# Performance work log

Hardware: AMD Instinct MI355X
Metric: run time of the kernel (lower is better)

## Reference

```python
import jax, jax.numpy as jnp
import numpy as np

S = 7          # number of slots
B = 8192       # batch
D = 1024       # input_dim
E = 256        # slot_embedding_dim
H = 512        # rnn_hidden_dim
SH = 256       # slot_hidden_dim
V = 100        # labels per slot (uniform)


def _lstm_cell(x, h, c, W_ih, W_hh, b_ih, b_hh):
    # PyTorch LSTMCell: gates ordered i, f, g, o
    gates = x @ W_ih.T + b_ih + h @ W_hh.T + b_hh
    i, f, g, o = jnp.split(gates, 4, axis=-1)
    i = jax.nn.sigmoid(i); f = jax.nn.sigmoid(f)
    g = jnp.tanh(g); o = jax.nn.sigmoid(o)
    c_new = f * c + i * g
    h_new = o * jnp.tanh(c_new)
    return h_new, c_new


def setup_inputs() -> dict:
    key = jax.random.key(0)
    ks = jax.random.split(key, 24)
    sc = 0.05
    D0 = D + E  # layer-0 input size
    inp = {
        'inputs': jax.random.normal(ks[0], (B, D), jnp.float32),
        'labels': jax.random.randint(ks[1], (S - 1, B), 0, V),
        'start': jax.random.normal(ks[2], (E,), jnp.float32),
        'emb': jax.random.normal(ks[3], (S - 1, V, E), jnp.float32) * sc,
        # layer 0 (input size D0)
        'W_ih0': jax.random.normal(ks[4], (S, 4 * H, D0), jnp.float32) * sc,
        'W_hh0': jax.random.normal(ks[5], (S, 4 * H, H), jnp.float32) * sc,
        'b_ih0': jax.random.normal(ks[6], (S, 4 * H), jnp.float32) * sc,
        'b_hh0': jax.random.normal(ks[7], (S, 4 * H), jnp.float32) * sc,
        'hwN_W0': jax.random.normal(ks[8], (S, H, D0 + H), jnp.float32) * sc,
        'hwN_b0': jax.random.normal(ks[9], (S, H), jnp.float32) * sc,
        'hwL_W0': jax.random.normal(ks[10], (S, H, D0), jnp.float32) * sc,
        # layer 1 (input size H)
        'W_ih1': jax.random.normal(ks[11], (S, 4 * H, H), jnp.float32) * sc,
        'W_hh1': jax.random.normal(ks[12], (S, 4 * H, H), jnp.float32) * sc,
        'b_ih1': jax.random.normal(ks[13], (S, 4 * H), jnp.float32) * sc,
        'b_hh1': jax.random.normal(ks[14], (S, 4 * H), jnp.float32) * sc,
        'hwN_W1': jax.random.normal(ks[15], (S, H, H + H), jnp.float32) * sc,
        'hwN_b1': jax.random.normal(ks[16], (S, H), jnp.float32) * sc,
        'hwL_W1': jax.random.normal(ks[17], (S, H, H), jnp.float32) * sc,
        # slot hidden + classifier
        'sh_W': jax.random.normal(ks[18], (S, SH, H), jnp.float32) * sc,
        'sh_b': jax.random.normal(ks[19], (S, SH), jnp.float32) * sc,
        'pred_W': jax.random.normal(ks[20], (S, V, SH), jnp.float32) * sc,
        'pred_b': jax.random.normal(ks[21], (S, V), jnp.float32) * sc,
    }
    return inp


def reference(inputs, labels, start, emb,
              W_ih0, W_hh0, b_ih0, b_hh0, hwN_W0, hwN_b0, hwL_W0,
              W_ih1, W_hh1, b_ih1, b_hh1, hwN_W1, hwN_b1, hwL_W1,
              sh_W, sh_b, pred_W, pred_b):
    bsz = inputs.shape[0]
    cur_emb = jnp.broadcast_to(start[None, :], (bsz, E))
    h0 = jnp.zeros((bsz, H), inputs.dtype); c0 = jnp.zeros((bsz, H), inputs.dtype)
    h1 = jnp.zeros((bsz, H), inputs.dtype); c1 = jnp.zeros((bsz, H), inputs.dtype)
    logits_all = []
    for i in range(S):  # slots are a short, structurally distinct recurrence
        x = jnp.concatenate([inputs, cur_emb], axis=-1)  # [B, D+E]
        # layer 0
        h0, c0 = _lstm_cell(x, h0, c0, W_ih0[i], W_hh0[i], b_ih0[i], b_hh0[i])
        gate = jax.nn.sigmoid(jnp.concatenate([x, h0], -1) @ hwN_W0[i].T + hwN_b0[i])
        cur = gate * h0 + (1.0 - gate) * (x @ hwL_W0[i].T)
        # layer 1
        h1, c1 = _lstm_cell(cur, h1, c1, W_ih1[i], W_hh1[i], b_ih1[i], b_hh1[i])
        gate1 = jax.nn.sigmoid(jnp.concatenate([cur, h1], -1) @ hwN_W1[i].T + hwN_b1[i])
        # (highway output of last layer feeds nothing further for this slot)
        _ = gate1 * h1 + (1.0 - gate1) * (cur @ hwL_W1[i].T)
        hidden = jax.nn.relu(h1 @ sh_W[i].T + sh_b[i])     # [B, SH]
        logits_all.append(hidden @ pred_W[i].T + pred_b[i])  # [B, V]
        if i < S - 1:
            cur_emb = emb[i][labels[i]]  # teacher-forced embedding lookup
    return jnp.stack(logits_all, axis=0)  # [S, B, V]
```

## Files before the change

kernel.cpp:

```cpp
#include <hip/hip_runtime.h>

#define SLOTS 7
#define BATCH 8192

typedef __attribute__((ext_vector_type(8))) __bf16 bf16x8;
typedef __attribute__((ext_vector_type(4))) float f32x4;

__device__ __forceinline__ void gl_lds16(const __bf16* g, __bf16* l) {
  __builtin_amdgcn_global_load_lds(
      (const __attribute__((address_space(1))) void*)g,
      (__attribute__((address_space(3))) void*)l, 16, 0, 0);
}

__device__ __forceinline__ float sigmoidf_(float x) {
  return 1.f / (1.f + __expf(-x));
}
__device__ __forceinline__ float tanhf_(float x) {
  float xc = fminf(fmaxf(x, -15.f), 15.f);
  float e = __expf(2.f * xc);
  return (e - 1.f) / (e + 1.f);
}

#define VMW(n) asm volatile("s_waitcnt vmcnt(" #n ")" ::: "memory")
#define BARF()                       \
  __builtin_amdgcn_s_barrier();      \
  asm volatile("" ::: "memory")

__global__ void __launch_bounds__(512, 2)
gemm8p(const __bf16* __restrict__ A, int lda,
       const __bf16* __restrict__ Bw, int ldb,
       const float* __restrict__ b_ih, const float* __restrict__ b_hh,
       float* __restrict__ cst, __bf16* __restrict__ hout, int hld, int hoff,
       float* __restrict__ auxw,
       int N, int NT, int NTaux, int Nreal) {
  extern __shared__ __bf16 lds[];
#define LDSH(b, s) (lds + (((b) << 2) + (s)) * 8192)
  const int tid = threadIdx.x;
  const int w = tid >> 6, lane = tid & 63;
  const int wr = w >> 2, wc = w & 3;
  const int ln = lane & 15, lh = lane >> 4;
  const int nbx = N >> 8;
  const int NB = gridDim.x;
  const int bid = blockIdx.x;
  const int wg = (bid & 7) * (NB >> 3) + (bid >> 3);
  const int bx = wg % nbx, by = wg / nbx;
  const int blockM = by << 8, blockN = bx << 8;
  const int nt = (blockN < Nreal) ? NT : NTaux;

  f32x4 acc[8][4];
#pragma unroll
  for (int i = 0; i < 8; ++i)
#pragma unroll
    for (int j = 0; j < 4; ++j) acc[i][j] = (f32x4){0.f, 0.f, 0.f, 0.f};

  auto stage = [&](int nb, int s, int kt) {
    const __bf16* base = (s & 1) ? Bw : A;
    const int ld = (s & 1) ? ldb : lda;
    const int rb = (s & 1) ? blockN : blockM;
    const int kh = s >> 1;
#pragma unroll
    for (int j = 0; j < 2; ++j) {
      const int c = j * 512 + w * 64 + lane;
      const int row = c >> 2;
      const int blklog = (c & 3) ^ ((c >> 3) & 3);
      const __bf16* src =
          base + (size_t)(rb + row) * ld + kt * 64 + kh * 32 + blklog * 8;
      gl_lds16(src, LDSH(nb, s) + j * 4096 + w * 512);
    }
  };

  bf16x8 a[8], bb[2];
  const int swz = ((lh ^ ((ln >> 1) & 3)) << 3);

#define RDA(slot)                                                            \
  {                                                                          \
    const __bf16* ap = LDSH(buf, slot);                                      \
    _Pragma("unroll") for (int mi = 0; mi < 8; ++mi) a[mi] =                 \
        *(const bf16x8*)&ap[(wr * 128 + mi * 16 + ln) * 32 + swz];           \
  }
#define RDB(slot, nh)                                                        \
  {                                                                          \
    const __bf16* bp = LDSH(buf, slot);                                      \
    _Pragma("unroll") for (int ni = 0; ni < 2; ++ni) bb[ni] =                \
        *(const bf16x8*)&bp[(wc * 64 + (nh)*32 + ni * 16 + ln) * 32 + swz];  \
  }
#define MFMA16(nh)                                                           \
  __builtin_amdgcn_s_setprio(1);                                             \
  _Pragma("unroll") for (int mi = 0; mi < 8; ++mi)                           \
      _Pragma("unroll") for (int ni = 0; ni < 2; ++ni)                       \
          acc[mi][(nh)*2 + ni] = __builtin_amdgcn_mfma_f32_16x16x32_bf16(    \
              a[mi], bb[ni], acc[mi][(nh)*2 + ni], 0, 0, 0);                 \
  __builtin_amdgcn_s_setprio(0);

#pragma unroll
  for (int s4 = 0; s4 < 4; ++s4) stage(0, s4, 0);
  VMW(4);
  BARF();

  int buf = 0;
  for (int t = 0; t < nt; ++t) {
    const int nb = buf ^ 1;
    const bool hn = (t + 1 < nt);
    RDA(0); RDB(1, 0);
    if (hn) stage(nb, 0, t + 1);
    MFMA16(0);
    RDB(1, 1);
    if (hn) stage(nb, 1, t + 1);
    MFMA16(1);
    if (hn) { VMW(4); } else { VMW(0); }
    BARF();
    RDA(2); RDB(3, 0);
    if (hn) stage(nb, 2, t + 1);
    MFMA16(0);
    RDB(3, 1);
    if (hn) stage(nb, 3, t + 1);
    MFMA16(1);
    if (hn) { VMW(4); }
    BARF();
    buf = nb;
  }
#undef RDA
#undef RDB
#undef MFMA16
#undef LDSH

  const int row0 = blockM + wr * 128 + (lh << 2);
  if (blockN < Nreal) {
    const int h = (((blockN >> 6) + wc) << 4) + ln;
    const float bs0 = b_ih[h] + b_hh[h];
    const float bs1 = b_ih[512 + h] + b_hh[512 + h];
    const float bs2 = b_ih[1024 + h] + b_hh[1024 + h];
    const float bs3 = b_ih[1536 + h] + b_hh[1536 + h];
#pragma unroll
    for (int mi = 0; mi < 8; ++mi)
#pragma unroll
      for (int r = 0; r < 4; ++r) {
        const int row = row0 + mi * 16 + r;
        float gi = sigmoidf_(acc[mi][0][r] + bs0);
        float gf = sigmoidf_(acc[mi][1][r] + bs1);
        float gg = tanhf_(acc[mi][2][r] + bs2);
        float go = sigmoidf_(acc[mi][3][r] + bs3);
        const size_t ci = (size_t)row * 512 + h;
        float cn = gf * cst[ci] + gi * gg;
        cst[ci] = cn;
        hout[(size_t)row * hld + hoff + h] = (__bf16)(go * tanhf_(cn));
      }
  } else {
#pragma unroll
    for (int mi = 0; mi < 8; ++mi)
#pragma unroll
      for (int n = 0; n < 4; ++n) {
        const int col = blockN - Nreal + wc * 64 + n * 16 + ln;
#pragma unroll
        for (int r = 0; r < 4; ++r)
          auxw[(size_t)(row0 + mi * 16 + r) * 1024 + col] = acc[mi][n][r];
      }
  }
}

template <int MODE>
__global__ void __launch_bounds__(256)
gemm_bt(const __bf16* __restrict__ A, int lda,
        const __bf16* __restrict__ Bw, int ldb,
        void* __restrict__ Cout, int ldc,
        const float* __restrict__ bias,
        const float* __restrict__ auxr,
        __bf16* __restrict__ hout, int hld, int hoff,
        const __bf16* __restrict__ hsrc,
        int M, int N, int K, int Nreal) {
  __shared__ __align__(16) __bf16 As[2][128 * 32];
  __shared__ __align__(16) __bf16 Bs[2][128 * 32];
  const int w = threadIdx.x >> 6;
  const int lane = threadIdx.x & 63;
  const int wr = w >> 1, wc = w & 1;
  const int rowBase = blockIdx.y << 7;
  const int colBase = blockIdx.x << 7;
  const int sr = lane >> 2;
  const int sc = (lane & 3) << 3;

  f32x4 acc[4][4];
#pragma unroll
  for (int i = 0; i < 4; ++i)
#pragma unroll
    for (int j = 0; j < 4; ++j) acc[i][j] = (f32x4){0.f, 0.f, 0.f, 0.f};

  const int nsteps = K >> 5;

#define STAGE(bi, k0)                                                           \
  {                                                                             \
    const __bf16* ga = A + (size_t)(rowBase + (w << 5) + sr) * lda + (k0) + sc; \
    gl_lds16(ga, &As[(bi)][(w << 5) * 32]);                                     \
    gl_lds16(ga + (size_t)16 * lda, &As[(bi)][((w << 5) + 16) * 32]);           \
    const __bf16* gb = Bw + (size_t)(colBase + (w << 5) + sr) * ldb + (k0) + sc;\
    gl_lds16(gb, &Bs[(bi)][(w << 5) * 32]);                                     \
    gl_lds16(gb + (size_t)16 * ldb, &Bs[(bi)][((w << 5) + 16) * 32]);           \
  }

  STAGE(0, 0);
  __syncthreads();
  int buf = 0;
  const int ln = lane & 15;
  const int kg = (lane >> 4) << 3;
  for (int t = 0; t < nsteps; ++t) {
    if (t + 1 < nsteps) STAGE(buf ^ 1, (t + 1) << 5);
    bf16x8 av[4], bv[4];
#pragma unroll
    for (int i = 0; i < 4; ++i)
      av[i] = *(const bf16x8*)&As[buf][((wr << 6) + (i << 4) + ln) * 32 + kg];
#pragma unroll
    for (int i = 0; i < 4; ++i)
      bv[i] = *(const bf16x8*)&Bs[buf][((wc << 6) + (i << 4) + ln) * 32 + kg];
#pragma unroll
    for (int mi = 0; mi < 4; ++mi)
#pragma unroll
      for (int ni = 0; ni < 4; ++ni)
        acc[mi][ni] = __builtin_amdgcn_mfma_f32_16x16x32_bf16(
            av[mi], bv[ni], acc[mi][ni], 0, 0, 0);
    __syncthreads();
    buf ^= 1;
  }
#undef STAGE

  const int lh = lane >> 4;
  const int row0 = rowBase + (wr << 6) + (lh << 2);
  const int col0 = colBase + (wc << 6) + ln;

  if (MODE == 1) {
    __bf16* C = (__bf16*)Cout;
#pragma unroll
    for (int mi = 0; mi < 4; ++mi)
#pragma unroll
      for (int ni = 0; ni < 4; ++ni) {
        const int col = col0 + (ni << 4);
        const float b = bias[col];
#pragma unroll
        for (int r = 0; r < 4; ++r) {
          float v = fmaxf(acc[mi][ni][r] + b, 0.f);
          C[(size_t)(row0 + (mi << 4) + r) * ldc + col] = (__bf16)v;
        }
      }
  } else if (MODE == 2) {
    float* C = (float*)Cout;
#pragma unroll
    for (int mi = 0; mi < 4; ++mi)
#pragma unroll
      for (int ni = 0; ni < 4; ++ni) {
        const int col = col0 + (ni << 4);
        if (col < Nreal) {
          const float b = bias[col];
#pragma unroll
          for (int r = 0; r < 4; ++r)
            C[(size_t)(row0 + (mi << 4) + r) * ldc + col] = acc[mi][ni][r] + b;
        }
      }
  } else if (MODE == 6) {
    __bf16* C = (__bf16*)Cout;
#pragma unroll
    for (int mi = 0; mi < 4; ++mi)
#pragma unroll
      for (int ni = 0; ni < 4; ++ni) {
        const int col = col0 + (ni << 4);
#pragma unroll
        for (int r = 0; r < 4; ++r) {
          const int row = row0 + (mi << 4) + r;
          float xp = auxr[(size_t)row * 1024 + col];
          float hwl = auxr[(size_t)row * 1024 + 512 + col];
          float gn = sigmoidf_(acc[mi][ni][r] + xp + bias[col]);
          float hn = (float)hsrc[(size_t)row * 512 + col];
          C[(size_t)row * ldc + col] = (__bf16)(gn * hn + (1.f - gn) * hwl);
          hout[(size_t)row * hld + hoff + col] = (__bf16)hn;
        }
      }
  }
}

__global__ void pack_w(const float* __restrict__ src, __bf16* __restrict__ dst,
                       int cols, int rows_s, int cols_s,
                       int sLd, int dLd, long dOff, int total) {
  int idx = blockIdx.x * 256 + threadIdx.x;
  if (idx >= total) return;
  int r = idx / cols;
  int c = idx - r * cols;
  float v = (r < rows_s && c < cols_s) ? src[(long)r * sLd + c] : 0.f;
  dst[dOff + (long)r * dLd + c] = (__bf16)v;
}

__global__ void pack_perm(const float* __restrict__ src, __bf16* __restrict__ dst,
                          int cols, int sLd, int dLd, long dColOff, int total) {
  int idx = blockIdx.x * 256 + threadIdx.x;
  if (idx >= total) return;
  int r = idx / cols;
  int c = idx - r * cols;
  int srcr = (((r >> 4) & 3) << 9) + ((r >> 6) << 4) + (r & 15);
  dst[(long)r * dLd + dColOff + c] = (__bf16)src[(long)srcr * sLd + c];
}

__global__ void conv_inputs(const float* __restrict__ in, __bf16* __restrict__ xh) {
  int idx = blockIdx.x * 256 + threadIdx.x;
  int b = idx >> 10, c = idx & 1023;
  xh[(size_t)b * 1792 + c] = (__bf16)in[idx];
}

__global__ void set_start(const float* __restrict__ start, __bf16* __restrict__ xh) {
  int idx = blockIdx.x * 256 + threadIdx.x;
  int b = idx >> 8, e = idx & 255;
  xh[(size_t)b * 1792 + 1024 + e] = (__bf16)start[e];
}

__global__ void emb_gather(const float* __restrict__ emb, const int* __restrict__ labels,
                           __bf16* __restrict__ xh) {
  int idx = blockIdx.x * 256 + threadIdx.x;
  int b = idx >> 8, e = idx & 255;
  int lab = labels[b];
  xh[(size_t)b * 1792 + 1024 + e] = (__bf16)emb[(size_t)lab * 256 + e];
}

__global__ void zero_states(__bf16* __restrict__ xh, __bf16* __restrict__ xh1A) {
  int idx = blockIdx.x * 256 + threadIdx.x;
  int b = idx >> 9, h = idx & 511;
  xh[(size_t)b * 1792 + 1280 + h] = (__bf16)0.f;
  xh1A[(size_t)b * 1024 + 512 + h] = (__bf16)0.f;
}

extern "C" void kernel_launch(void* const* d_in, const int* in_sizes, int n_in,
                              void* d_out, int out_size, void* d_ws, size_t ws_size,
                              hipStream_t stream) {
  const float* inputs = (const float*)d_in[0];
  const int* labels = (const int*)d_in[1];
  const float* start = (const float*)d_in[2];
  const float* emb = (const float*)d_in[3];
  const float* W_ih0 = (const float*)d_in[4];
  const float* W_hh0 = (const float*)d_in[5];
  const float* b_ih0 = (const float*)d_in[6];
  const float* b_hh0 = (const float*)d_in[7];
  const float* hwN_W0 = (const float*)d_in[8];
  const float* hwN_b0 = (const float*)d_in[9];
  const float* hwL_W0 = (const float*)d_in[10];
  const float* W_ih1 = (const float*)d_in[11];
  const float* W_hh1 = (const float*)d_in[12];
  const float* b_ih1 = (const float*)d_in[13];
  const float* b_hh1 = (const float*)d_in[14];
  const float* sh_W = (const float*)d_in[18];
  const float* sh_b = (const float*)d_in[19];
  const float* pred_W = (const float*)d_in[20];
  const float* pred_b = (const float*)d_in[21];
  float* out = (float*)d_out;

  char* p = (char*)d_ws;
  size_t off = 0;
  auto alloc = [&](size_t bytes) {
    void* r = p + off;
    off += (bytes + 255) & ~(size_t)255;
    return r;
  };
  __bf16* WA = (__bf16*)alloc((size_t)3072 * 1792 * 2);
  __bf16* WH = (__bf16*)alloc((size_t)512 * 512 * 2);
  __bf16* WB = (__bf16*)alloc((size_t)2048 * 1024 * 2);
  __bf16* WS = (__bf16*)alloc((size_t)256 * 512 * 2);
  __bf16* WP = (__bf16*)alloc((size_t)128 * 256 * 2);
  __bf16* xh = (__bf16*)alloc((size_t)BATCH * 1792 * 2);
  __bf16* xh1A = (__bf16*)alloc((size_t)BATCH * 1024 * 2);
  __bf16* xh1B = (__bf16*)alloc((size_t)BATCH * 1024 * 2);
  __bf16* h0new = (__bf16*)alloc((size_t)BATCH * 512 * 2);
  float* ghw = (float*)alloc((size_t)BATCH * 1024 * 4);
  float* c0 = (float*)alloc((size_t)BATCH * 512 * 4);
  float* c1 = (float*)alloc((size_t)BATCH * 512 * 4);
  __bf16* hidden = (__bf16*)ghw;
  (void)ws_size; (void)in_sizes; (void)n_in; (void)out_size;

  hipMemsetAsync(c0, 0, (size_t)BATCH * 512 * 4, stream);
  hipMemsetAsync(c1, 0, (size_t)BATCH * 512 * 4, stream);
  zero_states<<<BATCH * 512 / 256, 256, 0, stream>>>(xh, xh1A);
  conv_inputs<<<BATCH * 1024 / 256, 256, 0, stream>>>(inputs, xh);
  set_start<<<BATCH * 256 / 256, 256, 0, stream>>>(start, xh);

  const dim3 blk(256);
  for (int s = 0; s < SLOTS; ++s) {
    __bf16* xcur = (s & 1) ? xh1B : xh1A;
    __bf16* xnext = (s & 1) ? xh1A : xh1B;
    {
      int t;
      t = 2048 * 1280;
      pack_perm<<<(t + 255) / 256, blk, 0, stream>>>(
          W_ih0 + (size_t)s * 2048 * 1280, WA, 1280, 1280, 1792, 0, t);
      t = 2048 * 512;
      pack_perm<<<(t + 255) / 256, blk, 0, stream>>>(
          W_hh0 + (size_t)s * 2048 * 512, WA, 512, 512, 1792, 1280, t);
      t = 512 * 1792;
      pack_w<<<(t + 255) / 256, blk, 0, stream>>>(
          hwN_W0 + (size_t)s * 512 * 1792, WA, 1792, 512, 1280, 1792, 1792,
          (long)2048 * 1792, t);
      pack_w<<<(t + 255) / 256, blk, 0, stream>>>(
          hwL_W0 + (size_t)s * 512 * 1280, WA, 1792, 512, 1280, 1280, 1792,
          (long)2560 * 1792, t);
      t = 512 * 512;
      pack_w<<<(t + 255) / 256, blk, 0, stream>>>(
          hwN_W0 + (size_t)s * 512 * 1792 + 1280, WH, 512, 512, 512, 1792, 512, 0, t);
      t = 2048 * 512;
      pack_perm<<<(t + 255) / 256, blk, 0, stream>>>(
          W_ih1 + (size_t)s * 2048 * 512, WB, 512, 512, 1024, 0, t);
      pack_perm<<<(t + 255) / 256, blk, 0, stream>>>(
          W_hh1 + (size_t)s * 2048 * 512, WB, 512, 512, 1024, 512, t);
      t = 256 * 512;
      pack_w<<<(t + 255) / 256, blk, 0, stream>>>(
          sh_W + (size_t)s * 256 * 512, WS, 512, 256, 512, 512, 512, 0, t);
      t = 128 * 256;
      pack_w<<<(t + 255) / 256, blk, 0, stream>>>(
          pred_W + (size_t)s * 100 * 256, WP, 256, 100, 256, 256, 256, 0, t);
    }

    gemm8p<<<384, 512, 131072, stream>>>(
        xh, 1792, WA, 1792, b_ih0 + s * 2048, b_hh0 + s * 2048,
        c0, h0new, 512, 0, ghw, 3072, 28, 20, 2048);
    gemm_bt<6><<<dim3(4, 64), blk, 0, stream>>>(
        h0new, 512, WH, 512, xcur, 1024, hwN_b0 + s * 512,
        ghw, xh, 1792, 1280, h0new, BATCH, 512, 512, 512);
    if (s < SLOTS - 1)
      emb_gather<<<BATCH * 256 / 256, blk, 0, stream>>>(
          emb + (size_t)s * 100 * 256, labels + (size_t)s * BATCH, xh);
    gemm8p<<<256, 512, 131072, stream>>>(
        xcur, 1024, WB, 1024, b_ih1 + s * 2048, b_hh1 + s * 2048,
        c1, xnext, 1024, 512, nullptr, 2048, 16, 16, 2048);
    gemm_bt<1><<<dim3(2, 64), blk, 0, stream>>>(
        xnext + 512, 1024, WS, 512, hidden, 256, sh_b + s * 256,
        nullptr, nullptr, 0, 0, nullptr, BATCH, 256, 512, 256);
    gemm_bt<2><<<dim3(1, 64), blk, 0, stream>>>(
        hidden, 256, WP, 256, out + (size_t)s * BATCH * 100, 100,
        pred_b + s * 100, nullptr, nullptr, 0, 0, nullptr, BATCH, 128, 256, 100);
  }
}
```

Baseline: 1.730 ms.

## Split highway projections into separate GEMM and simplify gemm8p pipeline

```diff
diff --git a/kernel.cpp b/kernel.cpp
--- a/kernel.cpp
+++ b/kernel.cpp
@@ -31,8 +31,7 @@
        const __bf16* __restrict__ Bw, int ldb,
        const float* __restrict__ b_ih, const float* __restrict__ b_hh,
        float* __restrict__ cst, __bf16* __restrict__ hout, int hld, int hoff,
-       float* __restrict__ auxw,
-       int N, int NT, int NTaux, int Nreal) {
+       int N, int NT) {
   extern __shared__ __bf16 lds[];
 #define LDSH(b, s) (lds + (((b) << 2) + (s)) * 8192)
   const int tid = threadIdx.x;
@@ -45,7 +44,6 @@
   const int wg = (bid & 7) * (NB >> 3) + (bid >> 3);
   const int bx = wg % nbx, by = wg / nbx;
   const int blockM = by << 8, blockN = bx << 8;
-  const int nt = (blockN < Nreal) ? NT : NTaux;
 
   f32x4 acc[8][4];
 #pragma unroll
@@ -69,7 +67,7 @@
     }
   };
 
-  bf16x8 a[8], bb[2];
+  bf16x8 a[8], b0[2], b1[2];
   const int swz = ((lh ^ ((ln >> 1) & 3)) << 3);
 
 #define RDA(slot)                                                            \
@@ -78,84 +76,66 @@
     _Pragma("unroll") for (int mi = 0; mi < 8; ++mi) a[mi] =                 \
         *(const bf16x8*)&ap[(wr * 128 + mi * 16 + ln) * 32 + swz];           \
   }
-#define RDB(slot, nh)                                                        \
+#define RDB(slot)                                                            \
   {                                                                          \
     const __bf16* bp = LDSH(buf, slot);                                      \
-    _Pragma("unroll") for (int ni = 0; ni < 2; ++ni) bb[ni] =                \
-        *(const bf16x8*)&bp[(wc * 64 + (nh)*32 + ni * 16 + ln) * 32 + swz];  \
-  }
-#define MFMA16(nh)                                                           \
+    _Pragma("unroll") for (int ni = 0; ni < 2; ++ni) {                       \
+      b0[ni] = *(const bf16x8*)&bp[(wc * 64 + ni * 16 + ln) * 32 + swz];     \
+      b1[ni] = *(const bf16x8*)&bp[(wc * 64 + 32 + ni * 16 + ln) * 32 + swz];\
+    }                                                                        \
+  }
+#define MFMAC(bp, nh)                                                        \
   __builtin_amdgcn_s_setprio(1);                                             \
   _Pragma("unroll") for (int mi = 0; mi < 8; ++mi)                           \
       _Pragma("unroll") for (int ni = 0; ni < 2; ++ni)                       \
           acc[mi][(nh)*2 + ni] = __builtin_amdgcn_mfma_f32_16x16x32_bf16(    \
-              a[mi], bb[ni], acc[mi][(nh)*2 + ni], 0, 0, 0);                 \
+              a[mi], bp[ni], acc[mi][(nh)*2 + ni], 0, 0, 0);                 \
   __builtin_amdgcn_s_setprio(0);
 
 #pragma unroll
   for (int s4 = 0; s4 < 4; ++s4) stage(0, s4, 0);
-  VMW(4);
+  VMW(0);
   BARF();
 
   int buf = 0;
-  for (int t = 0; t < nt; ++t) {
+  for (int t = 0; t < NT; ++t) {
     const int nb = buf ^ 1;
-    const bool hn = (t + 1 < nt);
-    RDA(0); RDB(1, 0);
-    if (hn) stage(nb, 0, t + 1);
-    MFMA16(0);
-    RDB(1, 1);
-    if (hn) stage(nb, 1, t + 1);
-    MFMA16(1);
-    if (hn) { VMW(4); } else { VMW(0); }
-    BARF();
-    RDA(2); RDB(3, 0);
-    if (hn) stage(nb, 2, t + 1);
-    MFMA16(0);
-    RDB(3, 1);
-    if (hn) stage(nb, 3, t + 1);
-    MFMA16(1);
-    if (hn) { VMW(4); }
+    const bool hn = (t + 1 < NT);
+    RDA(0); RDB(1);
+    if (hn) { stage(nb, 0, t + 1); stage(nb, 1, t + 1); }
+    MFMAC(b0, 0); MFMAC(b1, 1);
+    RDA(2); RDB(3);
+    if (hn) { stage(nb, 2, t + 1); stage(nb, 3, t + 1); }
+    MFMAC(b0, 0); MFMAC(b1, 1);
+    VMW(0);
     BARF();
     buf = nb;
   }
 #undef RDA
 #undef RDB
-#undef MFMA16
+#undef MFMAC
 #undef LDSH
 
   const int row0 = blockM + wr * 128 + (lh << 2);
-  if (blockN < Nreal) {
-    const int h = (((blockN >> 6) + wc) << 4) + ln;
-    const float bs0 = b_ih[h] + b_hh[h];
-    const float bs1 = b_ih[512 + h] + b_hh[512 + h];
-    const float bs2 = b_ih[1024 + h] + b_hh[1024 + h];
-    const float bs3 = b_ih[1536 + h] + b_hh[1536 + h];
-#pragma unroll
-    for (int mi = 0; mi < 8; ++mi)
-#pragma unroll
-      for (int r = 0; r < 4; ++r) {
-        const int row = row0 + mi * 16 + r;
-        float gi = sigmoidf_(acc[mi][0][r] + bs0);
-        float gf = sigmoidf_(acc[mi][1][r] + bs1);
-        float gg = tanhf_(acc[mi][2][r] + bs2);
-        float go = sigmoidf_(acc[mi][3][r] + bs3);
-        const size_t ci = (size_t)row * 512 + h;
-        float cn = gf * cst[ci] + gi * gg;
-        cst[ci] = cn;
-        hout[(size_t)row * hld + hoff + h] = (__bf16)(go * tanhf_(cn));
-      }
-  } else {
-#pragma unroll
-    for (int mi = 0; mi < 8; ++mi)
-#pragma unroll
-      for (int n = 0; n < 4; ++n) {
-        const int col = blockN - Nreal + wc * 64 + n * 16 + ln;
-#pragma unroll
-        for (int r = 0; r < 4; ++r)
-          auxw[(size_t)(row0 + mi * 16 + r) * 1024 + col] = acc[mi][n][r];
-      }
-  }
+  const int h = (((blockN >> 6) + wc) << 4) + ln;
+  const float bs0 = b_ih[h] + b_hh[h];
+  const float bs1 = b_ih[512 + h] + b_hh[512 + h];
+  const float bs2 = b_ih[1024 + h] + b_hh[1024 + h];
+  const float bs3 = b_ih[1536 + h] + b_hh[1536 + h];
+#pragma unroll
+  for (int mi = 0; mi < 8; ++mi)
+#pragma unroll
+    for (int r = 0; r < 4; ++r) {
+      const int row = row0 + mi * 16 + r;
+      float gi = sigmoidf_(acc[mi][0][r] + bs0);
+      float gf = sigmoidf_(acc[mi][1][r] + bs1);
+      float gg = tanhf_(acc[mi][2][r] + bs2);
+      float go = sigmoidf_(acc[mi][3][r] + bs3);
+      const size_t ci = (size_t)row * 512 + h;
+      float cn = gf * cst[ci] + gi * gg;
+      cst[ci] = cn;
+      hout[(size_t)row * hld + hoff + h] = (__bf16)(go * tanhf_(cn));
+    }
 }
 
 template <int MODE>
@@ -225,7 +205,18 @@
   const int row0 = rowBase + (wr << 6) + (lh << 2);
   const int col0 = colBase + (wc << 6) + ln;
 
-  if (MODE == 1) {
+  if (MODE == 0) {
+    float* C = (float*)Cout;
+#pragma unroll
+    for (int mi = 0; mi < 4; ++mi)
+#pragma unroll
+      for (int ni = 0; ni < 4; ++ni) {
+        const int col = col0 + (ni << 4);
+#pragma unroll
+        for (int r = 0; r < 4; ++r)
+          C[(size_t)(row0 + (mi << 4) + r) * ldc + col] = acc[mi][ni][r];
+      }
+  } else if (MODE == 1) {
     __bf16* C = (__bf16*)Cout;
 #pragma unroll
     for (int mi = 0; mi < 4; ++mi)
@@ -353,7 +344,8 @@
     off += (bytes + 255) & ~(size_t)255;
     return r;
   };
-  __bf16* WA = (__bf16*)alloc((size_t)3072 * 1792 * 2);
+  __bf16* WA = (__bf16*)alloc((size_t)2048 * 1792 * 2);
+  __bf16* WX = (__bf16*)alloc((size_t)1024 * 1280 * 2);
   __bf16* WH = (__bf16*)alloc((size_t)512 * 512 * 2);
   __bf16* WB = (__bf16*)alloc((size_t)2048 * 1024 * 2);
   __bf16* WS = (__bf16*)alloc((size_t)256 * 512 * 2);
@@ -386,13 +378,12 @@
       t = 2048 * 512;
       pack_perm<<<(t + 255) / 256, blk, 0, stream>>>(
           W_hh0 + (size_t)s * 2048 * 512, WA, 512, 512, 1792, 1280, t);
-      t = 512 * 1792;
+      t = 512 * 1280;
       pack_w<<<(t + 255) / 256, blk, 0, stream>>>(
-          hwN_W0 + (size_t)s * 512 * 1792, WA, 1792, 512, 1280, 1792, 1792,
-          (long)2048 * 1792, t);
+          hwN_W0 + (size_t)s * 512 * 1792, WX, 1280, 512, 1280, 1792, 1280, 0, t);
       pack_w<<<(t + 255) / 256, blk, 0, stream>>>(
-          hwL_W0 + (size_t)s * 512 * 1280, WA, 1792, 512, 1280, 1280, 1792,
-          (long)2560 * 1792, t);
+          hwL_W0 + (size_t)s * 512 * 1280, WX, 1280, 512, 1280, 1280, 1280,
+          (long)512 * 1280, t);
       t = 512 * 512;
       pack_w<<<(t + 255) / 256, blk, 0, stream>>>(
           hwN_W0 + (size_t)s * 512 * 1792 + 1280, WH, 512, 512, 512, 1792, 512, 0, t);
@@ -409,9 +400,12 @@
           pred_W + (size_t)s * 100 * 256, WP, 256, 100, 256, 256, 256, 0, t);
     }
 
-    gemm8p<<<384, 512, 131072, stream>>>(
+    gemm_bt<0><<<dim3(8, 64), blk, 0, stream>>>(
+        xh, 1792, WX, 1280, ghw, 1024, nullptr,
+        nullptr, nullptr, 0, 0, nullptr, BATCH, 1024, 1280, 1024);
+    gemm8p<<<256, 512, 131072, stream>>>(
         xh, 1792, WA, 1792, b_ih0 + s * 2048, b_hh0 + s * 2048,
-        c0, h0new, 512, 0, ghw, 3072, 28, 20, 2048);
+        c0, h0new, 512, 0, 2048, 28);
     gemm_bt<6><<<dim3(4, 64), blk, 0, stream>>>(
         h0new, 512, WH, 512, xcur, 1024, hwN_b0 + s * 512,
         ghw, xh, 1792, 1280, h0new, BATCH, 512, 512, 512);
@@ -420,7 +414,7 @@
           emb + (size_t)s * 100 * 256, labels + (size_t)s * BATCH, xh);
     gemm8p<<<256, 512, 131072, stream>>>(
         xcur, 1024, WB, 1024, b_ih1 + s * 2048, b_hh1 + s * 2048,
-        c1, xnext, 1024, 512, nullptr, 2048, 16, 16, 2048);
+        c1, xnext, 1024, 512, 2048, 16);
     gemm_bt<1><<<dim3(2, 64), blk, 0, stream>>>(
         xnext + 512, 1024, WS, 512, hidden, 256, sh_b + s * 256,
         nullptr, nullptr, 0, 0, nullptr, BATCH, 256, 512, 256);
```

New measurement: 1.655 ms. -4.3%, faster.
